# Performance work log

Measured on AMD Instinct MI355X. Metric: run time of the kernel, lower is better.

## Reference

```python
import jax, jax.numpy as jnp
import numpy as np

B, H, W, C = 32, 32, 32, 256
AD, RR = 8, 16
DN = ('NHWC', 'HWIO', 'NHWC')


def _conv(a, w, dil=1, groups=1):
    return jax.lax.conv_general_dilated(a, w, (1, 1), 'SAME', rhs_dilation=(dil, dil),
                                        dimension_numbers=DN, feature_group_count=groups)


def _branch(a, w1, b1, dw, pw, b3, wd, bd):
    # (Conv1x1 + SeparableConv3x3 + DilatedConv3x3), each sigmoid-activated, averaged
    y1 = jax.nn.sigmoid(_conv(a, w1) + b1)
    y3 = jax.nn.sigmoid(_conv(_conv(a, dw, groups=a.shape[-1]), pw) + b3)  # depthwise (no bias) -> pointwise
    yd = jax.nn.sigmoid(_conv(a, wd, dil=2) + bd)
    return (y1 + y3 + yd) / 3.0


def setup_inputs() -> dict:
    key = jax.random.key(0)
    ks = iter(jax.random.split(key, 64))
    nrm = lambda shape, s=0.05: jax.random.normal(next(ks), shape, jnp.float32) * s
    d = {'x': jax.random.normal(next(ks), (B, H, W, C), jnp.float32)}
    for p in ('cc', 'ch', 'cw'):
        d[p + '1_w'] = nrm((1, 1, C, 1)); d[p + '1_b'] = jnp.zeros((1,), jnp.float32)
        d[p + '3_dw'] = nrm((3, 3, 1, C)); d[p + '3_pw'] = nrm((1, 1, C, 1)); d[p + '3_b'] = jnp.zeros((1,), jnp.float32)
        d[p + 'd_w'] = nrm((3, 3, C, 1)); d[p + 'd_b'] = jnp.zeros((1,), jnp.float32)
    d['branch_w'] = jax.random.uniform(next(ks), (3,), jnp.float32, -0.05, 0.05)
    d['d1_w'] = nrm((C, RR)); d['d1_b'] = jnp.zeros((RR,), jnp.float32)
    d['d2_w'] = nrm((RR, 1)); d['d2_b'] = jnp.zeros((1,), jnp.float32)
    for p in ('q', 'k', 'v'):
        d[p + '_w'] = nrm((1, 1, 3, AD)); d[p + '_b'] = jnp.zeros((AD,), jnp.float32)
    d['o_w'] = nrm((1, 1, AD, 1)); d['o_b'] = jnp.zeros((1,), jnp.float32)
    d['gamma'] = jnp.ones((H, W, C), jnp.float32)
    d['beta'] = jnp.zeros((H, W, C), jnp.float32)
    return d


def reference(x, cc1_w, cc1_b, cc3_dw, cc3_pw, cc3_b, ccd_w, ccd_b,
              ch1_w, ch1_b, ch3_dw, ch3_pw, ch3_b, chd_w, chd_b,
              cw1_w, cw1_b, cw3_dw, cw3_pw, cw3_b, cwd_w, cwd_b,
              branch_w, d1_w, d1_b, d2_w, d2_b,
              q_w, q_b, k_w, k_b, v_w, v_b, o_w, o_b, gamma, beta):
    Bx, Hx, Wx, Cx = x.shape
    # global SE context: GAP -> Dense(relu) -> Dense(sigmoid) -> broadcast over H,W
    g = jnp.mean(x, axis=(1, 2), keepdims=True)                       # [B,1,1,C]
    g = jax.nn.relu(g @ d1_w + d1_b)
    g = jax.nn.sigmoid(g @ d2_w + d2_b)                               # [B,1,1,1]
    # channel branch: mean over H,W -> convs over [B,1,1,C] -> scalar gate
    ca = _branch(jnp.mean(x, axis=(1, 2), keepdims=True), cc1_w, cc1_b, cc3_dw, cc3_pw, cc3_b, ccd_w, ccd_b)  # [B,1,1,1]
    x_c = x * ca
    # height branch: mean over W -> [B,1,H,C] -> convs -> [B,1,H,1] -> gate per-H
    ha_in = jnp.transpose(jnp.mean(x, axis=2, keepdims=True), (0, 2, 1, 3))
    ha = _branch(ha_in, ch1_w, ch1_b, ch3_dw, ch3_pw, ch3_b, chd_w, chd_b)
    x_h = x * jnp.transpose(ha, (0, 2, 1, 3))                         # [B,H,1,1] broadcast
    # width branch: mean over H -> [B,1,W,C] -> convs -> [B,1,W,1] -> gate per-W
    wa = _branch(jnp.mean(x, axis=1, keepdims=True), cw1_w, cw1_b, cw3_dw, cw3_pw, cw3_b, cwd_w, cwd_b)
    x_w = x * wa
    bw = jax.nn.softmax(branch_w)
    combined = bw[0] * x_c + bw[1] * x_h + bw[2] * x_w
    # small self-attention over the 3 channel-mean maps
    maps = jnp.concatenate([jnp.mean(x_c, axis=-1, keepdims=True),
                            jnp.mean(x_h, axis=-1, keepdims=True),
                            jnp.mean(x_w, axis=-1, keepdims=True)], axis=-1)  # [B,H,W,3]
    Q = (jnp.einsum('bhwc,co->bhwo', maps, q_w[0, 0]) + q_b).reshape(Bx, Hx * Wx, AD)
    K = (jnp.einsum('bhwc,co->bhwo', maps, k_w[0, 0]) + k_b).reshape(Bx, Hx * Wx, AD)
    V = (jnp.einsum('bhwc,co->bhwo', maps, v_w[0, 0]) + v_b).reshape(Bx, Hx * Wx, AD)
    att = jax.nn.softmax(jnp.einsum('bnd,bmd->bnm', Q, K) / jnp.sqrt(jnp.float32(AD)), axis=-1)
    ao = jnp.einsum('bnm,bmd->bnd', att, V).reshape(Bx, Hx, Wx, AD)
    cross = jax.nn.sigmoid(jnp.einsum('bhwd,do->bhwo', ao, o_w[0, 0]) + o_b)  # [B,H,W,1]
    y = combined * cross * g + x
    # LayerNorm over (H,W,C) per sample, keras eps=1e-3
    mu = jnp.mean(y, axis=(1, 2, 3), keepdims=True)
    var = jnp.mean((y - mu) ** 2, axis=(1, 2, 3), keepdims=True)
    return (y - mu) / jnp.sqrt(var + 1e-3) * gamma + beta
```

## Files before the change

kernel.cpp:

```cpp
#include <hip/hip_runtime.h>


#define B_   32
#define H_   32
#define W_   32
#define C_   256
#define N_   1024
#define HWC_ (32*32*256)

#define OFF_XW    0
#define OFF_XH    262144
#define OFF_MC    524288
#define OFF_M2    557056
#define OFF_T     589824
#define OFF_HA    622592
#define OFF_WA    623616
#define OFF_CA    624640
#define OFF_G     624672
#define OFF_CST   624704
#define OFF_LNP   624736
#define WS_FLOATS 628832

#define NCOPY   8
#define CSTRIDE 1028

__device__ __forceinline__ float sigm_(float v){ return 1.f/(1.f + __expf(-v)); }
__device__ __forceinline__ float dot4_(float4 a, float4 b){
  return a.x*b.x + a.y*b.y + a.z*b.z + a.w*b.w;
}

__global__ __launch_bounds__(256) void kAB(const float* __restrict__ x, float* __restrict__ ws){
  __shared__ float4 sl4[256];
  const int blk = blockIdx.x;
  const int tid = threadIdx.x, lane = tid & 63, wv = tid >> 6;
  if (blk < 1024){
    const int b = blk >> 5, h = blk & 31;
    const float* xp = x + (size_t)(b*H_ + h)*(W_*C_);
    float4 v[8];
    #pragma unroll
    for (int k = 0; k < 8; ++k) v[k] = ((const float4*)xp)[tid + k*256];
    #pragma unroll
    for (int k = 0; k < 8; ++k){
      float s = v[k].x + v[k].y + v[k].z + v[k].w;
      float q = v[k].x*v[k].x + v[k].y*v[k].y + v[k].z*v[k].z + v[k].w*v[k].w;
      #pragma unroll
      for (int d = 1; d < 64; d <<= 1){ s += __shfl_xor(s, d); q += __shfl_xor(q, d); }
      if (lane == 0){
        const int w = k*4 + wv;
        ws[OFF_MC + b*N_ + h*W_ + w] = s * (1.f/C_);
        ws[OFF_M2 + b*N_ + h*W_ + w] = q;
      }
    }
    float4 a = v[0];
    #pragma unroll
    for (int k = 1; k < 8; ++k){ a.x += v[k].x; a.y += v[k].y; a.z += v[k].z; a.w += v[k].w; }
    sl4[tid] = a;
    __syncthreads();
    if (tid < 64){
      const float4 p0 = sl4[tid], p1 = sl4[tid+64], p2 = sl4[tid+128], p3 = sl4[tid+192];
      float4 o;
      o.x = (p0.x+p1.x+p2.x+p3.x)*(1.f/W_);
      o.y = (p0.y+p1.y+p2.y+p3.y)*(1.f/W_);
      o.z = (p0.z+p1.z+p2.z+p3.z)*(1.f/W_);
      o.w = (p0.w+p1.w+p2.w+p3.w)*(1.f/W_);
      ((float4*)(ws + OFF_XW + (b*H_ + h)*C_))[tid] = o;
    }
  } else {
    const int blk2 = blk - 1024, b = blk2 >> 5, w = blk2 & 31;
    const int hh = tid >> 6, c4 = (tid & 63)*4;
    const float* xp = x + (size_t)b*HWC_ + (size_t)w*C_ + c4;
    float4 acc = {0.f,0.f,0.f,0.f};
    #pragma unroll
    for (int hb = 0; hb < 8; ++hb){
      const int h = hb*4 + hh;
      const float4 v = *(const float4*)(xp + (size_t)h*(W_*C_));
      acc.x += v.x; acc.y += v.y; acc.z += v.z; acc.w += v.w;
    }
    sl4[tid] = acc;
    __syncthreads();
    if (tid < 64){
      const float4 a = sl4[tid], b2 = sl4[tid+64], c = sl4[tid+128], d = sl4[tid+192];
      float4 o;
      o.x = (a.x+b2.x+c.x+d.x)*(1.f/H_);
      o.y = (a.y+b2.y+c.y+d.y)*(1.f/H_);
      o.z = (a.z+b2.z+c.z+d.z)*(1.f/H_);
      o.w = (a.w+b2.w+c.w+d.w)*(1.f/H_);
      *(float4*)&ws[OFF_XH + (b*W_ + w)*C_ + tid*4] = o;
    }
  }
}

__global__ __launch_bounds__(256) void kC(float* __restrict__ ws,
  const float* __restrict__ cc1_w, const float* __restrict__ cc1_b, const float* __restrict__ cc3_dw,
  const float* __restrict__ cc3_pw, const float* __restrict__ cc3_b, const float* __restrict__ ccd_w, const float* __restrict__ ccd_b,
  const float* __restrict__ ch1_w, const float* __restrict__ ch1_b, const float* __restrict__ ch3_dw,
  const float* __restrict__ ch3_pw, const float* __restrict__ ch3_b, const float* __restrict__ chd_w, const float* __restrict__ chd_b,
  const float* __restrict__ cw1_w, const float* __restrict__ cw1_b, const float* __restrict__ cw3_dw,
  const float* __restrict__ cw3_pw, const float* __restrict__ cw3_b, const float* __restrict__ cwd_w, const float* __restrict__ cwd_b,
  const float* __restrict__ branch_w, const float* __restrict__ d1_w, const float* __restrict__ d1_b,
  const float* __restrict__ d2_w, const float* __restrict__ d2_b,
  const float* __restrict__ q_w, const float* __restrict__ q_b, const float* __restrict__ k_w, const float* __restrict__ k_b,
  const float* __restrict__ v_w, const float* __restrict__ v_b, const float* __restrict__ o_w, const float* __restrict__ o_b)
{
  const int b = blockIdx.x, y = blockIdx.y;
  const int tid = threadIdx.x, lane = tid & 63, wv = tid >> 6;

  if (y < 16){
    const int prof = y >> 3;
    const int h = ((y & 7) << 2) | wv;
    const float* P  = ws + (prof ? OFF_XH : OFF_XW) + b*(32*C_);
    const float* w1 = prof ? cw1_w  : ch1_w;
    const float* b1 = prof ? cw1_b  : ch1_b;
    const float* dw = prof ? cw3_dw : ch3_dw;
    const float* pw = prof ? cw3_pw : ch3_pw;
    const float* b3 = prof ? cw3_b  : ch3_b;
    const float* wd = prof ? cwd_w  : chd_w;
    const float* bd = prof ? cwd_b  : chd_b;
    const int c4 = lane*4;
    const float4 z4 = {0.f,0.f,0.f,0.f};
    const float4 r0  = *(const float4*)(P + h*C_ + c4);
    const float4 rm1 = (h > 0)  ? *(const float4*)(P + (h-1)*C_ + c4) : z4;
    const float4 rp1 = (h < 31) ? *(const float4*)(P + (h+1)*C_ + c4) : z4;
    const float4 rm2 = (h > 1)  ? *(const float4*)(P + (h-2)*C_ + c4) : z4;
    const float4 rp2 = (h < 30) ? *(const float4*)(P + (h+2)*C_ + c4) : z4;
    const float4 w1q = *(const float4*)(w1 + c4);
    const float4 d3  = *(const float4*)(dw + 3*C_ + c4);
    const float4 d4  = *(const float4*)(dw + 4*C_ + c4);
    const float4 d5  = *(const float4*)(dw + 5*C_ + c4);
    const float4 pwq = *(const float4*)(pw + c4);
    const float4 g3  = *(const float4*)(wd + 3*C_ + c4);
    const float4 g4  = *(const float4*)(wd + 4*C_ + c4);
    const float4 g5  = *(const float4*)(wd + 5*C_ + c4);
    float s1 = dot4_(r0, w1q);
    float4 dv;
    dv.x = rm1.x*d3.x + r0.x*d4.x + rp1.x*d5.x;
    dv.y = rm1.y*d3.y + r0.y*d4.y + rp1.y*d5.y;
    dv.z = rm1.z*d3.z + r0.z*d4.z + rp1.z*d5.z;
    dv.w = rm1.w*d3.w + r0.w*d4.w + rp1.w*d5.w;
    float s3 = dot4_(dv, pwq);
    float sd = (rm2.x*g3.x + r0.x*g4.x + rp2.x*g5.x)
             + (rm2.y*g3.y + r0.y*g4.y + rp2.y*g5.y)
             + (rm2.z*g3.z + r0.z*g4.z + rp2.z*g5.z)
             + (rm2.w*g3.w + r0.w*g4.w + rp2.w*g5.w);
    #pragma unroll
    for (int d = 1; d < 64; d <<= 1){ s1 += __shfl_xor(s1,d); s3 += __shfl_xor(s3,d); sd += __shfl_xor(sd,d); }
    if (lane == 0)
      ws[(prof ? OFF_WA : OFF_HA) + b*32 + h] =
          (sigm_(s1 + b1[0]) + sigm_(s3 + b3[0]) + sigm_(sd + bd[0])) * (1.f/3.f);
    return;
  }

  __shared__ float gvec[C_];
  { float s = 0.f;
    const float* P = ws + OFF_XW + b*(32*C_);
    #pragma unroll
    for (int h = 0; h < H_; ++h) s += P[h*C_ + tid];
    gvec[tid] = s * (1.f/H_); }
  __syncthreads();

  if (wv == 0){
    float s1 = 0.f, s3 = 0.f, sd = 0.f;
    #pragma unroll
    for (int k = 0; k < 4; ++k){
      const int c = lane + k*64;
      const float v = gvec[c];
      s1 = fmaf(v, cc1_w[c], s1);
      s3 = fmaf(v*cc3_dw[4*C_+c], cc3_pw[c], s3);
      sd = fmaf(v, ccd_w[4*C_+c], sd);
    }
    #pragma unroll
    for (int d = 1; d < 64; d <<= 1){ s1 += __shfl_xor(s1,d); s3 += __shfl_xor(s3,d); sd += __shfl_xor(sd,d); }
    if (lane == 0)
      ws[OFF_CA + b] = (sigm_(s1+cc1_b[0]) + sigm_(s3+cc3_b[0]) + sigm_(sd+ccd_b[0])) * (1.f/3.f);
  } else if (wv == 1){
    float acc = 0.f;
    for (int r = 0; r < 16; ++r){
      float s = 0.f;
      #pragma unroll
      for (int k = 0; k < 4; ++k){ const int c = lane + k*64; s = fmaf(gvec[c], d1_w[c*16 + r], s); }
      #pragma unroll
      for (int d = 1; d < 64; d <<= 1) s += __shfl_xor(s, d);
      acc = fmaf(fmaxf(s + d1_b[r], 0.f), d2_w[r], acc);
    }
    if (lane == 0) ws[OFF_G + b] = sigm_(acc + d2_b[0]);
  } else if (wv == 2 && b == 0){
    if (lane < 16){
      const int i = lane >> 2, j = lane & 3;
      float s = 0.f;
      #pragma unroll
      for (int d = 0; d < 8; ++d){
        const float qv = (i < 3) ? q_w[i*8+d] : q_b[d];
        const float kv = (j < 3) ? k_w[j*8+d] : k_b[d];
        s = fmaf(qv, kv, s);
      }
      ws[OFF_CST + i*4 + j] = s * 0.51010305898f;
    } else if (lane < 19){
      const int i = lane - 16;
      float s = 0.f;
      #pragma unroll
      for (int d = 0; d < 8; ++d) s = fmaf(v_w[i*8+d], o_w[d], s);
      ws[OFF_CST + lane] = s;
    } else if (lane == 19){
      float s = o_b[0];
      #pragma unroll
      for (int d = 0; d < 8; ++d) s = fmaf(v_b[d], o_w[d], s);
      ws[OFF_CST + 19] = s;
    } else if (lane == 20){
      const float b0 = branch_w[0], b1 = branch_w[1], b2 = branch_w[2];
      const float mx = fmaxf(b0, fmaxf(b1, b2));
      const float e0 = __expf(b0-mx), e1 = __expf(b1-mx), e2 = __expf(b2-mx);
      const float inv = 1.f/(e0+e1+e2);
      ws[OFF_CST+20] = e0*inv; ws[OFF_CST+21] = e1*inv; ws[OFF_CST+22] = e2*inv;
      ws[OFF_CST+23] = 0.f;
    }
  }
}

#define ATT1(MV, WV) do{                       \
    const float vv = fmaf(p2, (WV), th);       \
    const float ss = fmaf((MV), vv, p3);       \
    const float ee = exp2f(ss);                \
    Z += ee;                                   \
    const float em = ee * (MV);                \
    semc += em;                                \
    A2 = fmaf(em, (WV), A2);                   \
  }while(0)

__global__ __launch_bounds__(256, 4) void kD(float* __restrict__ ws){
  __shared__ __align__(16) float mcs[NCOPY*CSTRIDE];
  __shared__ float ha_s[32], wa_s[32], cst[24], sc[2], red[8];
  const int blk = blockIdx.x, b = blk >> 6, rblk = blk & 63;
  const int tid = threadIdx.x, lane = tid & 63, wv = tid >> 6;
  const int r = tid >> 4, sub = tid & 15;
  const int n = rblk*16 + r;

  const float4 v  = ((const float4*)(ws + OFF_MC + b*N_))[tid];
  const float m2v = ws[OFF_M2 + b*N_ + n];
  const float mcn = ws[OFF_MC + b*N_ + n];
  if (tid < 32){ ha_s[tid] = ws[OFF_HA + b*32 + tid]; wa_s[tid] = ws[OFF_WA + b*32 + tid]; }
  else if (tid >= 64 && tid < 88) cst[tid-64] = ws[OFF_CST + (tid-64)];
  else if (tid == 96){ sc[0] = ws[OFF_CA + b]; sc[1] = ws[OFF_G + b]; }
  #pragma unroll
  for (int cp = 0; cp < NCOPY; ++cp) *(float4*)&mcs[cp*CSTRIDE + tid*4] = v;
  __syncthreads();

  const float ca = sc[0], gg = sc[1];
  const int hn = n >> 5, wn = n & 31;
  const float u0 = mcn*ca, u1 = mcn*ha_s[hn], u2 = mcn*wa_s[wn];
  const float p0 = u0*cst[0] + u1*cst[4] + u2*cst[8]  + cst[12];
  const float p1 = u0*cst[1] + u1*cst[5] + u2*cst[9]  + cst[13];
  const float p2 = u0*cst[2] + u1*cst[6] + u2*cst[10] + cst[14];
  const float p3 = u0*cst[3] + u1*cst[7] + u2*cst[11] + cst[15];
  const float pc = p0 * ca;

  float Z = 0.f, A0 = 0.f, A1 = 0.f, A2 = 0.f;
  const float* mrow_base = &mcs[(sub & 7)*CSTRIDE];
  #pragma unroll
  for (int j = 0; j < 2; ++j){
    const int hm = sub*2 + j;
    const float th = fmaf(p1, ha_s[hm], pc);
    float semc = 0.f;
    const float* mrow = mrow_base + hm*32;
    #pragma unroll
    for (int wm = 0; wm < 32; wm += 4){
      const float4 m4 = *(const float4*)&mrow[wm];
      const float4 w4 = *(const float4*)&wa_s[wm];
      ATT1(m4.x, w4.x);
      ATT1(m4.y, w4.y);
      ATT1(m4.z, w4.z);
      ATT1(m4.w, w4.w);
    }
    A0 += semc; A1 = fmaf(ha_s[hm], semc, A1);
  }
  #pragma unroll
  for (int d = 1; d < 16; d <<= 1){
    Z  += __shfl_xor(Z, d);
    A0 += __shfl_xor(A0, d);
    A1 += __shfl_xor(A1, d);
    A2 += __shfl_xor(A2, d);
  }

  float t1 = 0.f, t2 = 0.f;
  if (sub == 0){
    const float invZ = 1.f / Z;
    const float dot = (ca*cst[16]*A0 + cst[17]*A1 + cst[18]*A2) * invZ + cst[19];
    const float cross = 1.f / (1.f + __expf(-dot));
    const float S = cst[20]*ca + cst[21]*ha_s[hn] + cst[22]*wa_s[wn];
    const float T = fmaf(S*cross, gg, 1.f);
    ws[OFF_T + b*N_ + n] = T;
    t1 = T * mcn * (float)C_;
    t2 = T * T * m2v;
  }
  #pragma unroll
  for (int d = 1; d < 64; d <<= 1){ t1 += __shfl_xor(t1,d); t2 += __shfl_xor(t2,d); }
  if (lane == 0){ red[wv] = t1; red[4+wv] = t2; }
  __syncthreads();
  if (tid == 0){
    ws[OFF_LNP + (b*64 + rblk)*2 + 0] = red[0]+red[1]+red[2]+red[3];
    ws[OFF_LNP + (b*64 + rblk)*2 + 1] = red[4]+red[5]+red[6]+red[7];
  }
}

__global__ __launch_bounds__(256) void kF(const float* __restrict__ x, const float* __restrict__ gamma,
                                          const float* __restrict__ beta, const float* __restrict__ ws,
                                          float* __restrict__ out){
  const int blk = blockIdx.x, b = blk >> 5, h = blk & 31;
  const int tid = threadIdx.x;
  __shared__ float a1s[32];
  __shared__ float mu_r[2];
  if (tid == 0){
    float s1 = 0.f, s2 = 0.f;
    for (int i = 0; i < 64; ++i){
      s1 += ws[OFF_LNP + (b*64+i)*2 + 0];
      s2 += ws[OFF_LNP + (b*64+i)*2 + 1];
    }
    const float mu  = s1 * (1.f/HWC_);
    const float var = s2 * (1.f/HWC_) - mu*mu;
    const float rstd = rsqrtf(var + 1e-3f);
    mu_r[0] = mu * rstd; mu_r[1] = rstd;
  }
  __syncthreads();
  if (tid < 32) a1s[tid] = ws[OFF_T + b*N_ + h*32 + tid] * mu_r[1];
  __syncthreads();
  const float murstd = mu_r[0];
  const size_t base = (size_t)(b*H_ + h)*(W_*C_);
  const float4* xp = (const float4*)(x + base);
  const float4* gp = (const float4*)(gamma + (size_t)h*(W_*C_));
  const float4* bp = (const float4*)(beta  + (size_t)h*(W_*C_));
  float4* op = (float4*)(out + base);
  #pragma unroll
  for (int k = 0; k < 8; ++k){
    const int f = tid + k*256;
    const float a1 = a1s[f >> 6];
    const float4 xv = xp[f], gv = gp[f], bv = bp[f];
    float4 o;
    o.x = fmaf(fmaf(xv.x, a1, -murstd), gv.x, bv.x);
    o.y = fmaf(fmaf(xv.y, a1, -murstd), gv.y, bv.y);
    o.z = fmaf(fmaf(xv.z, a1, -murstd), gv.z, bv.z);
    o.w = fmaf(fmaf(xv.w, a1, -murstd), gv.w, bv.w);
    op[f] = o;
  }
}

extern "C" void kernel_launch(void* const* d_in, const int* in_sizes, int n_in,
                              void* d_out, int out_size, void* d_ws, size_t ws_size,
                              hipStream_t stream){
  (void)in_sizes; (void)n_in; (void)out_size;
  if (ws_size < (size_t)WS_FLOATS * sizeof(float)) return;
  const float* x      = (const float*)d_in[0];
  const float* cc1_w  = (const float*)d_in[1];
  const float* cc1_b  = (const float*)d_in[2];
  const float* cc3_dw = (const float*)d_in[3];
  const float* cc3_pw = (const float*)d_in[4];
  const float* cc3_b  = (const float*)d_in[5];
  const float* ccd_w  = (const float*)d_in[6];
  const float* ccd_b  = (const float*)d_in[7];
  const float* ch1_w  = (const float*)d_in[8];
  const float* ch1_b  = (const float*)d_in[9];
  const float* ch3_dw = (const float*)d_in[10];
  const float* ch3_pw = (const float*)d_in[11];
  const float* ch3_b  = (const float*)d_in[12];
  const float* chd_w  = (const float*)d_in[13];
  const float* chd_b  = (const float*)d_in[14];
  const float* cw1_w  = (const float*)d_in[15];
  const float* cw1_b  = (const float*)d_in[16];
  const float* cw3_dw = (const float*)d_in[17];
  const float* cw3_pw = (const float*)d_in[18];
  const float* cw3_b  = (const float*)d_in[19];
  const float* cwd_w  = (const float*)d_in[20];
  const float* cwd_b  = (const float*)d_in[21];
  const float* branch_w = (const float*)d_in[22];
  const float* d1_w   = (const float*)d_in[23];
  const float* d1_b   = (const float*)d_in[24];
  const float* d2_w   = (const float*)d_in[25];
  const float* d2_b   = (const float*)d_in[26];
  const float* q_w    = (const float*)d_in[27];
  const float* q_b    = (const float*)d_in[28];
  const float* k_w    = (const float*)d_in[29];
  const float* k_b    = (const float*)d_in[30];
  const float* v_w    = (const float*)d_in[31];
  const float* v_b    = (const float*)d_in[32];
  const float* o_w    = (const float*)d_in[33];
  const float* o_b    = (const float*)d_in[34];
  const float* gamma  = (const float*)d_in[35];
  const float* beta   = (const float*)d_in[36];
  float* ws = (float*)d_ws;
  float* out = (float*)d_out;

  kAB<<<dim3(2048), dim3(256), 0, stream>>>(x, ws);
  kC<<<dim3(B_, 17), dim3(256), 0, stream>>>(ws,
      cc1_w, cc1_b, cc3_dw, cc3_pw, cc3_b, ccd_w, ccd_b,
      ch1_w, ch1_b, ch3_dw, ch3_pw, ch3_b, chd_w, chd_b,
      cw1_w, cw1_b, cw3_dw, cw3_pw, cw3_b, cwd_w, cwd_b,
      branch_w, d1_w, d1_b, d2_w, d2_b,
      q_w, q_b, k_w, k_b, v_w, v_b, o_w, o_b);
  kD<<<dim3(B_*64), dim3(256), 0, stream>>>(ws);
  kF<<<dim3(B_*H_), dim3(256), 0, stream>>>(x, gamma, beta, ws, out);
}
```

Measured before the change: 50.57 us.

## Precompute per-key value projection in shared memory to shrink attention inner loop

```diff
diff --git a/kernel.cpp b/kernel.cpp
--- a/kernel.cpp
+++ b/kernel.cpp
@@ -21,8 +21,14 @@
 #define OFF_LNP   624736
 #define WS_FLOATS 628832
 
-#define NCOPY   8
+#define NCOPY   4
 #define CSTRIDE 1028
+
+#if __has_builtin(__builtin_amdgcn_exp2f)
+#define EXP2F(x) __builtin_amdgcn_exp2f(x)
+#else
+#define EXP2F(x) exp2f(x)
+#endif
 
 __device__ __forceinline__ float sigm_(float v){ return 1.f/(1.f + __expf(-v)); }
 __device__ __forceinline__ float dot4_(float4 a, float4 b){
@@ -173,16 +179,17 @@
     if (lane == 0)
       ws[OFF_CA + b] = (sigm_(s1+cc1_b[0]) + sigm_(s3+cc3_b[0]) + sigm_(sd+ccd_b[0])) * (1.f/3.f);
   } else if (wv == 1){
-    float acc = 0.f;
-    for (int r = 0; r < 16; ++r){
-      float s = 0.f;
-      #pragma unroll
-      for (int k = 0; k < 4; ++k){ const int c = lane + k*64; s = fmaf(gvec[c], d1_w[c*16 + r], s); }
-      #pragma unroll
-      for (int d = 1; d < 64; d <<= 1) s += __shfl_xor(s, d);
-      acc = fmaf(fmaxf(s + d1_b[r], 0.f), d2_w[r], acc);
-    }
-    if (lane == 0) ws[OFF_G + b] = sigm_(acc + d2_b[0]);
+    const int r16 = lane & 15, cg = lane >> 4;
+    float s = 0.f;
+    #pragma unroll
+    for (int i = 0; i < 64; ++i){
+      const int c = cg*64 + i;
+      s = fmaf(gvec[c], d1_w[c*16 + r16], s);
+    }
+    s += __shfl_xor(s, 16); s += __shfl_xor(s, 32);
+    float t = fmaxf(s + d1_b[r16], 0.f) * d2_w[r16];
+    t += __shfl_xor(t, 1); t += __shfl_xor(t, 2); t += __shfl_xor(t, 4); t += __shfl_xor(t, 8);
+    if (lane == 0) ws[OFF_G + b] = sigm_(t + d2_b[0]);
   } else if (wv == 2 && b == 0){
     if (lane < 16){
       const int i = lane >> 2, j = lane & 3;
@@ -216,23 +223,15 @@
   }
 }
 
-#define ATT1(MV, WV) do{                       \
-    const float vv = fmaf(p2, (WV), th);       \
-    const float ss = fmaf((MV), vv, p3);       \
-    const float ee = exp2f(ss);                \
-    Z += ee;                                   \
-    const float em = ee * (MV);                \
-    semc += em;                                \
-    A2 = fmaf(em, (WV), A2);                   \
-  }while(0)
-
 __global__ __launch_bounds__(256, 4) void kD(float* __restrict__ ws){
   __shared__ __align__(16) float mcs[NCOPY*CSTRIDE];
+  __shared__ __align__(16) float qs [NCOPY*CSTRIDE];
   __shared__ float ha_s[32], wa_s[32], cst[24], sc[2], red[8];
   const int blk = blockIdx.x, b = blk >> 6, rblk = blk & 63;
   const int tid = threadIdx.x, lane = tid & 63, wv = tid >> 6;
   const int r = tid >> 4, sub = tid & 15;
   const int n = rblk*16 + r;
+  const int hn = n >> 5, wn = n & 31;
 
   const float4 v  = ((const float4*)(ws + OFF_MC + b*N_))[tid];
   const float m2v = ws[OFF_M2 + b*N_ + n];
@@ -245,7 +244,20 @@
   __syncthreads();
 
   const float ca = sc[0], gg = sc[1];
-  const int hn = n >> 5, wn = n & 31;
+  {
+    const int hm0 = tid >> 3;
+    const int wm0 = (tid*4) & 31;
+    const float base = ca*cst[16] + cst[17]*ha_s[hm0];
+    float4 q;
+    q.x = v.x * (base + cst[18]*wa_s[wm0+0]);
+    q.y = v.y * (base + cst[18]*wa_s[wm0+1]);
+    q.z = v.z * (base + cst[18]*wa_s[wm0+2]);
+    q.w = v.w * (base + cst[18]*wa_s[wm0+3]);
+    #pragma unroll
+    for (int cp = 0; cp < NCOPY; ++cp) *(float4*)&qs[cp*CSTRIDE + tid*4] = q;
+  }
+  __syncthreads();
+
   const float u0 = mcn*ca, u1 = mcn*ha_s[hn], u2 = mcn*wa_s[wn];
   const float p0 = u0*cst[0] + u1*cst[4] + u2*cst[8]  + cst[12];
   const float p1 = u0*cst[1] + u1*cst[5] + u2*cst[9]  + cst[13];
@@ -253,37 +265,35 @@
   const float p3 = u0*cst[3] + u1*cst[7] + u2*cst[11] + cst[15];
   const float pc = p0 * ca;
 
-  float Z = 0.f, A0 = 0.f, A1 = 0.f, A2 = 0.f;
-  const float* mrow_base = &mcs[(sub & 7)*CSTRIDE];
+  float Z = 0.f, ACC = 0.f;
+  const float* mbase = &mcs[(sub & 3)*CSTRIDE];
+  const float* qbase = &qs [(sub & 3)*CSTRIDE];
   #pragma unroll
   for (int j = 0; j < 2; ++j){
     const int hm = sub*2 + j;
     const float th = fmaf(p1, ha_s[hm], pc);
-    float semc = 0.f;
-    const float* mrow = mrow_base + hm*32;
+    const float* mrow = mbase + hm*32;
+    const float* qrow = qbase + hm*32;
     #pragma unroll
     for (int wm = 0; wm < 32; wm += 4){
       const float4 m4 = *(const float4*)&mrow[wm];
+      const float4 q4 = *(const float4*)&qrow[wm];
       const float4 w4 = *(const float4*)&wa_s[wm];
-      ATT1(m4.x, w4.x);
-      ATT1(m4.y, w4.y);
-      ATT1(m4.z, w4.z);
-      ATT1(m4.w, w4.w);
-    }
-    A0 += semc; A1 = fmaf(ha_s[hm], semc, A1);
+      { const float vv = fmaf(p2, w4.x, th); const float ee = EXP2F(fmaf(m4.x, vv, p3)); Z += ee; ACC = fmaf(ee, q4.x, ACC); }
+      { const float vv = fmaf(p2, w4.y, th); const float ee = EXP2F(fmaf(m4.y, vv, p3)); Z += ee; ACC = fmaf(ee, q4.y, ACC); }
+      { const float vv = fmaf(p2, w4.z, th); const float ee = EXP2F(fmaf(m4.z, vv, p3)); Z += ee; ACC = fmaf(ee, q4.z, ACC); }
+      { const float vv = fmaf(p2, w4.w, th); const float ee = EXP2F(fmaf(m4.w, vv, p3)); Z += ee; ACC = fmaf(ee, q4.w, ACC); }
+    }
   }
   #pragma unroll
   for (int d = 1; d < 16; d <<= 1){
-    Z  += __shfl_xor(Z, d);
-    A0 += __shfl_xor(A0, d);
-    A1 += __shfl_xor(A1, d);
-    A2 += __shfl_xor(A2, d);
+    Z   += __shfl_xor(Z, d);
+    ACC += __shfl_xor(ACC, d);
   }
 
   float t1 = 0.f, t2 = 0.f;
   if (sub == 0){
-    const float invZ = 1.f / Z;
-    const float dot = (ca*cst[16]*A0 + cst[17]*A1 + cst[18]*A2) * invZ + cst[19];
+    const float dot = ACC / Z + cst[19];
     const float cross = 1.f / (1.f + __expf(-dot));
     const float S = cst[20]*ca + cst[21]*ha_s[hn] + cst[22]*wa_s[wn];
     const float T = fmaf(S*cross, gg, 1.f);
```

After: 46.98 us. 1.08x faster.
